# Optimization experiments

Measured on AMD Instinct MI355X. Metric: run time of the kernel, lower is better.

The kernel has to match this reference:

```python
import jax, jax.numpy as jnp
import numpy as np


def setup_inputs() -> dict:
    key = jax.random.key(0)
    k1, k2 = jax.random.split(key)
    B, S, V = 256, 4096, 128000
    input_ids = jax.random.randint(k1, (B, S), 0, V, dtype=jnp.int32)
    last_token_index = jax.random.randint(k2, (B, 1), 0, S, dtype=jnp.int32)
    return {"input_ids": input_ids, "last_token_index": last_token_index, "vocab_size": V}


def reference(input_ids, last_token_index, vocab_size):
    # token_count[b, v] = #{ s : s < last_token_index[b] and input_ids[b, s] == v }
    B, S = input_ids.shape
    # positions >= last_token_index are invalid: remap to vocab_size (out of range -> dropped)
    valid = jnp.arange(S, dtype=jnp.int32)[None, :] < last_token_index  # (B, S)
    used_tokens = jnp.where(valid, input_ids, jnp.int32(vocab_size))    # (B, S)
    token_count = jnp.zeros((B, vocab_size), dtype=jnp.int32)
    # batched scatter-add histogram; out-of-range index vocab_size is dropped
    token_count = token_count.at[jnp.arange(B, dtype=jnp.int32)[:, None], used_tokens].add(
        jnp.int32(1), mode="drop")
    return token_count
```

## Files before the change

### kernel.cpp

```cpp
#include <hip/hip_runtime.h>


#define NB      256
#define SLEN    4096
#define VOC     128000
#define THREADS 512
#define PART_BINS   16000
#define WORDS   (PART_BINS/2)
#define NXCD    8

typedef int vint4 __attribute__((ext_vector_type(4)));

#define LDS_BARRIER() do {                                   \
    asm volatile("s_waitcnt lgkmcnt(0)" ::: "memory");       \
    __builtin_amdgcn_s_barrier();                            \
    __builtin_amdgcn_sched_barrier(0);                       \
} while (0)

__global__ __launch_bounds__(THREADS) void fused_hist_kernel(
    const int* __restrict__ input_ids,
    const int* __restrict__ last_token_index,
    int* __restrict__ out)
{
    __shared__ int lds[WORDS];

    const int i    = blockIdx.x;
    const int xcd  = i & (NXCD - 1);
    const int j    = i >> 3;
    const int b    = xcd * (NB / NXCD) + (j >> 2);
    const int q    = j & 3;

    const int* __restrict__ row_in = input_ids + (size_t)b * SLEN;
    int* __restrict__ out_row      = out + (size_t)b * VOC;

    const int L = last_token_index[b];

    vint4 t[2];
#pragma unroll
    for (int k = 0; k < 2; ++k) {
        const int v4 = threadIdx.x + k * THREADS;
        const int s0 = v4 * 4;
        vint4 w = { 0x40000000, 0x40000000, 0x40000000, 0x40000000 };
        if (s0 < L) {
            w = reinterpret_cast<const vint4*>(row_in)[v4];
            if (s0 + 1 >= L) w.y = 0x40000000;
            if (s0 + 2 >= L) w.z = 0x40000000;
            if (s0 + 3 >= L) w.w = 0x40000000;
        }
        t[k] = w;
    }

#pragma unroll
    for (int sp = 0; sp < 2; ++sp) {
        const int part = 2 * q + sp;
        const int lo   = part * PART_BINS;

        if (sp != 0) LDS_BARRIER();

        {
            vint4 z = { 0, 0, 0, 0 };
            vint4* __restrict__ l4 = reinterpret_cast<vint4*>(lds);
            for (int k = threadIdx.x; k < WORDS / 4; k += THREADS) {
                l4[k] = z;
            }
        }
        LDS_BARRIER();

#pragma unroll
        for (int k = 0; k < 2; ++k) {
            const int tok[4] = { t[k].x, t[k].y, t[k].z, t[k].w };
#pragma unroll
            for (int e = 0; e < 4; ++e) {
                const unsigned d = (unsigned)(tok[e] - lo);
                if (d < (unsigned)PART_BINS) {
                    atomicAdd(&lds[d >> 1], 1 << ((d & 1) * 16));
                }
            }
        }
        LDS_BARRIER();

        {
            const int2* __restrict__ src = reinterpret_cast<const int2*>(lds);
            vint4* __restrict__ dst = reinterpret_cast<vint4*>(out_row + lo);
            for (int k = threadIdx.x; k < PART_BINS / 4; k += THREADS) {
                int2 w = src[k];
                vint4 o;
                o.x = w.x & 0xFFFF;
                o.y = (int)((unsigned)w.x >> 16);
                o.z = w.y & 0xFFFF;
                o.w = (int)((unsigned)w.y >> 16);
                dst[k] = o;
            }
        }
    }
}

extern "C" void kernel_launch(void* const* d_in, const int* in_sizes, int n_in,
                              void* d_out, int out_size, void* d_ws, size_t ws_size,
                              hipStream_t stream) {
    const int* input_ids        = (const int*)d_in[0];
    const int* last_token_index = (const int*)d_in[1];
    int* out = (int*)d_out;

    fused_hist_kernel<<<dim3(1024), dim3(THREADS), 0, stream>>>(
        input_ids, last_token_index, out);
}
```

Measured before the change: 24.08 us.

## Double-buffer LDS histogram partitions to overlap zeroing with global stores

Halves the LDS partition size and uses two ping-pong LDS buffers, so each block now handles four smaller sub-partitions instead of two. The next buffer is zeroed while the current one is written out to global memory, which cuts one barrier phase per partition and lets zeroing overlap the store traffic. In exchange, every block re-scans its tokens four times instead of twice, paying more compare and atomic passes, and runs more barrier rounds. LDS use per block is unchanged.

```diff
diff --git a/kernel.cpp b/kernel.cpp
--- a/kernel.cpp
+++ b/kernel.cpp
@@ -5,8 +5,9 @@
 #define SLEN    4096
 #define VOC     128000
 #define THREADS 512
-#define PART_BINS   16000
+#define PART_BINS   8000
 #define WORDS   (PART_BINS/2)
+#define NSP     4
 #define NXCD    8
 
 typedef int vint4 __attribute__((ext_vector_type(4)));
@@ -17,12 +18,55 @@
     __builtin_amdgcn_sched_barrier(0);                       \
 } while (0)
 
+__device__ __forceinline__ void zero_buf(int* buf) {
+    vint4 z = { 0, 0, 0, 0 };
+    vint4* l4 = reinterpret_cast<vint4*>(buf);
+#pragma unroll
+    for (int k = 0; k < WORDS / 4; k += THREADS) {
+        const int idx = k + threadIdx.x;
+        if (idx < WORDS / 4) l4[idx] = z;
+    }
+}
+
+__device__ __forceinline__ void scatter_buf(int* buf, const vint4* t, int lo) {
+#pragma unroll
+    for (int k = 0; k < 2; ++k) {
+        const int tok[4] = { t[k].x, t[k].y, t[k].z, t[k].w };
+#pragma unroll
+        for (int e = 0; e < 4; ++e) {
+            const unsigned d = (unsigned)(tok[e] - lo);
+            if (d < (unsigned)PART_BINS) {
+                atomicAdd(&buf[d >> 1], 1 << ((d & 1) * 16));
+            }
+        }
+    }
+}
+
+__device__ __forceinline__ void store_buf(const int* buf, int* dst_row) {
+    const int2* src = reinterpret_cast<const int2*>(buf);
+    vint4* dst = reinterpret_cast<vint4*>(dst_row);
+#pragma unroll
+    for (int k = 0; k < PART_BINS / 4; k += THREADS) {
+        const int idx = k + threadIdx.x;
+        if (idx < PART_BINS / 4) {
+            int2 w = src[idx];
+            vint4 o;
+            o.x = w.x & 0xFFFF;
+            o.y = (int)((unsigned)w.x >> 16);
+            o.z = w.y & 0xFFFF;
+            o.w = (int)((unsigned)w.y >> 16);
+            dst[idx] = o;
+        }
+    }
+}
+
 __global__ __launch_bounds__(THREADS) void fused_hist_kernel(
     const int* __restrict__ input_ids,
     const int* __restrict__ last_token_index,
     int* __restrict__ out)
 {
-    __shared__ int lds[WORDS];
+    __shared__ int lds0[WORDS];
+    __shared__ int lds1[WORDS];
 
     const int i    = blockIdx.x;
     const int xcd  = i & (NXCD - 1);
@@ -50,47 +94,25 @@
         t[k] = w;
     }
 
+    const int base_lo = (q * NSP) * PART_BINS;
+
+    zero_buf(lds0);
+    LDS_BARRIER();
+    scatter_buf(lds0, t, base_lo);
+    LDS_BARRIER();
+
 #pragma unroll
-    for (int sp = 0; sp < 2; ++sp) {
-        const int part = 2 * q + sp;
-        const int lo   = part * PART_BINS;
+    for (int sp = 0; sp < NSP; ++sp) {
+        int* cur = (sp & 1) ? lds1 : lds0;
+        int* nxt = (sp & 1) ? lds0 : lds1;
 
-        if (sp != 0) LDS_BARRIER();
-
-        {
-            vint4 z = { 0, 0, 0, 0 };
-            vint4* __restrict__ l4 = reinterpret_cast<vint4*>(lds);
-            for (int k = threadIdx.x; k < WORDS / 4; k += THREADS) {
-                l4[k] = z;
-            }
-        }
+        if (sp + 1 < NSP) zero_buf(nxt);
+        store_buf(cur, out_row + base_lo + sp * PART_BINS);
         LDS_BARRIER();
 
-#pragma unroll
-        for (int k = 0; k < 2; ++k) {
-            const int tok[4] = { t[k].x, t[k].y, t[k].z, t[k].w };
-#pragma unroll
-            for (int e = 0; e < 4; ++e) {
-                const unsigned d = (unsigned)(tok[e] - lo);
-                if (d < (unsigned)PART_BINS) {
-                    atomicAdd(&lds[d >> 1], 1 << ((d & 1) * 16));
-                }
-            }
-        }
-        LDS_BARRIER();
-
-        {
-            const int2* __restrict__ src = reinterpret_cast<const int2*>(lds);
-            vint4* __restrict__ dst = reinterpret_cast<vint4*>(out_row + lo);
-            for (int k = threadIdx.x; k < PART_BINS / 4; k += THREADS) {
-                int2 w = src[k];
-                vint4 o;
-                o.x = w.x & 0xFFFF;
-                o.y = (int)((unsigned)w.x >> 16);
-                o.z = w.y & 0xFFFF;
-                o.w = (int)((unsigned)w.y >> 16);
-                dst[k] = o;
-            }
+        if (sp + 1 < NSP) {
+            scatter_buf(nxt, t, base_lo + (sp + 1) * PART_BINS);
+            LDS_BARRIER();
         }
     }
 }
```

Result: no change. 23.84 us (-1.0%).
